# Optimization experiments

Measured on AMD Instinct MI355X. Metric: run time of the kernel, lower is better.

## Reference

```python
import jax, jax.numpy as jnp
import numpy as np

# LeNet-5 C3 connectivity table: which of the 6 input maps feed each of the 16 output maps.
MAP_S2 = [[0, 1, 2], [1, 2, 3], [2, 3, 4], [3, 4, 5], [0, 4, 5], [0, 1, 5],
          [0, 1, 2, 3], [1, 2, 3, 4], [2, 3, 4, 5], [0, 3, 4, 5], [0, 1, 4, 5],
          [0, 1, 2, 5], [0, 1, 3, 4], [1, 2, 4, 5], [0, 2, 3, 5], [0, 1, 2, 3, 4, 5]]

_mask_np = np.zeros((16, 6), dtype=np.float32)
for i, conn in enumerate(MAP_S2):
    _mask_np[i, conn] = 1.0
CONN_MASK = jnp.asarray(_mask_np)  # [out_ch=16, in_ch=6]


def setup_inputs() -> dict:
    key = jax.random.key(0)
    kx, kw, kb = jax.random.split(key, 3)
    x = jax.random.normal(kx, (32, 6, 512, 512), dtype=jnp.float32)
    # Dense weight; unconnected (out,in) pairs are masked to zero in reference(),
    # matching the per-output-channel gather + tiny conv of the original module.
    weight = jax.random.normal(kw, (16, 6, 5, 5), dtype=jnp.float32) * 0.1
    bias = jax.random.normal(kb, (16,), dtype=jnp.float32) * 0.1
    return {"x": x, "weight": weight, "bias": bias}


def reference(x, weight, bias):
    # Mask enforces the sparse channel connectivity: equivalent to gathering
    # each output map's input-channel subset and running a tiny 5x5 conv.
    w = weight * CONN_MASK[:, :, None, None]  # [16,6,5,5]
    out = jax.lax.conv_general_dilated(
        x, w,
        window_strides=(1, 1), padding='VALID',
        dimension_numbers=('NCHW', 'OIHW', 'NCHW'))
    return out + bias[None, :, None, None]  # [B,16,H-4,W-4]
```

## Files before the change

### kernel.cpp

```cpp
#include <hip/hip_runtime.h>


#define TILE_W 64
#define TILE_H 16
#define IN_W   (TILE_W + 4)
#define IN_H   (TILE_H + 4)

__global__ __launch_bounds__(256, 3) void c3_kernel(
    const float* __restrict__ x, const float* __restrict__ wgt,
    const float* __restrict__ bias, float* __restrict__ out)
{
    constexpr int IC = 6, OC = 16, H = 512, W = 512, OH = 508, OW = 508;
    static constexpr int CONN[6][10] = {
        {0, 4, 5, 6, 9, 10, 11, 12, 14, 15},
        {0, 1, 5, 6, 7, 10, 11, 12, 13, 15},
        {0, 1, 2, 6, 7, 8, 11, 13, 14, 15},
        {1, 2, 3, 6, 7, 8, 9, 12, 14, 15},
        {2, 3, 4, 7, 8, 9, 10, 12, 13, 15},
        {3, 4, 5, 8, 9, 10, 11, 13, 14, 15}};

    __shared__ __align__(16) float xs[IC][IN_H][IN_W];
    __shared__ __align__(16) float ws[IC][5][OC][8];

    const int tid = threadIdx.x;
    const int ow0 = blockIdx.x * TILE_W;
    const int oh0 = blockIdx.y * TILE_H;
    const int n   = blockIdx.z;

    for (int i = tid; i < OC * IC * 25; i += 256) {
        const int oc = i / 150;
        const int rem = i % 150;
        const int ic = rem / 25;
        const int kh = (rem % 25) / 5;
        const int kw = rem % 5;
        ws[ic][kh][oc][kw] = wgt[i];
    }

    const float* xn = x + (size_t)n * IC * H * W;
    for (int i = tid; i < IC * IN_H * (IN_W / 4); i += 256) {
        const int ic  = i / (IN_H * 17);
        const int rem = i % (IN_H * 17);
        const int r   = rem / 17;
        const int c4  = (rem % 17) * 4;
        int h = oh0 + r; if (h > H - 1) h = H - 1;
        const int wc = ow0 + c4;
        float4 v;
        if (wc <= W - 4) {
            v = *(const float4*)(xn + ((size_t)ic * H + h) * W + wc);
        } else {
            v = make_float4(0.f, 0.f, 0.f, 0.f);
        }
        *(float4*)&xs[ic][r][c4] = v;
    }
    __syncthreads();

    const int row = tid >> 4;
    const int c0  = (tid & 15) * 4;

    float acc[OC][4];
    #pragma unroll
    for (int oc = 0; oc < OC; ++oc)
        #pragma unroll
        for (int r = 0; r < 4; ++r) acc[oc][r] = 0.f;

    #pragma unroll 1
    for (int kh = 0; kh < 5; ++kh) {
        #pragma unroll
        for (int ic = 0; ic < IC; ++ic) {
            float in[8];
            *(float4*)&in[0] = *(const float4*)&xs[ic][row + kh][c0];
            *(float4*)&in[4] = *(const float4*)&xs[ic][row + kh][c0 + 4];
            #pragma unroll
            for (int j = 0; j < 10; ++j) {
                const int oc = CONN[ic][j];
                float wv[5];
                *(float4*)&wv[0] = *(const float4*)&ws[ic][kh][oc][0];
                wv[4] = ws[ic][kh][oc][4];
                #pragma unroll
                for (int kw = 0; kw < 5; ++kw)
                    #pragma unroll
                    for (int r = 0; r < 4; ++r)
                        acc[oc][r] = fmaf(in[r + kw], wv[kw], acc[oc][r]);
            }
        }
    }

    const int oh = oh0 + row;
    const int ow = ow0 + c0;
    if (oh < OH && ow < OW) {
        float* op = out + (((size_t)n * OC) * OH + oh) * OW + ow;
        #pragma unroll
        for (int oc = 0; oc < OC; ++oc) {
            const float b = bias[oc];
            float4 v = make_float4(acc[oc][0] + b, acc[oc][1] + b,
                                   acc[oc][2] + b, acc[oc][3] + b);
            *(float4*)(op + (size_t)oc * OH * OW) = v;
        }
    }
}

extern "C" void kernel_launch(void* const* d_in, const int* in_sizes, int n_in,
                              void* d_out, int out_size, void* d_ws, size_t ws_size,
                              hipStream_t stream) {
    const float* x    = (const float*)d_in[0];
    const float* wgt  = (const float*)d_in[1];
    const float* bias = (const float*)d_in[2];
    float* out = (float*)d_out;
    dim3 grid((508 + TILE_W - 1) / TILE_W,
              (508 + TILE_H - 1) / TILE_H,
              32);
    c3_kernel<<<grid, dim3(256), 0, stream>>>(x, wgt, bias, out);
}
```

Before: 965.0 us.

## Repack sparse weights in a prelaunch kernel and read them as uniform scalar loads

Adds a small one-block kernel that repacks only the connected weights into a contiguous per-(ic,kh) layout in workspace. The main kernel then reads weights straight from global memory with wave-uniform addresses, which should lower to scalar loads, instead of staging all weights in LDS. This drops the LDS weight buffer and its per-FMA LDS reads, and raises the occupancy hint to 4 blocks per CU. In exchange it adds an extra kernel launch and relies on the scalar cache for weight fetches.

```diff
diff --git a/kernel.cpp b/kernel.cpp
--- a/kernel.cpp
+++ b/kernel.cpp
@@ -6,35 +6,46 @@
 #define IN_W   (TILE_W + 4)
 #define IN_H   (TILE_H + 4)
 
-__global__ __launch_bounds__(256, 3) void c3_kernel(
-    const float* __restrict__ x, const float* __restrict__ wgt,
+#define CONN_TABLE {                              \
+    {0, 4, 5, 6, 9, 10, 11, 12, 14, 15},          \
+    {0, 1, 5, 6, 7, 10, 11, 12, 13, 15},          \
+    {0, 1, 2, 6, 7, 8, 11, 13, 14, 15},           \
+    {1, 2, 3, 6, 7, 8, 9, 12, 14, 15},            \
+    {2, 3, 4, 7, 8, 9, 10, 12, 13, 15},           \
+    {3, 4, 5, 8, 9, 10, 11, 13, 14, 15}}
+
+__global__ __launch_bounds__(256) void c3_repack(
+    const float* __restrict__ wgt, float* __restrict__ rp)
+{
+    static constexpr int CONN[6][10] = CONN_TABLE;
+    for (int idx = threadIdx.x; idx < 6 * 5 * 64; idx += 256) {
+        const int blk  = idx >> 6;
+        const int slot = idx & 63;
+        const int ic = blk / 5, kh = blk % 5;
+        float v = 0.f;
+        if (slot < 50) {
+            const int j = slot / 5, kw = slot % 5;
+            const int oc = CONN[ic][j];
+            v = wgt[((oc * 6 + ic) * 5 + kh) * 5 + kw];
+        }
+        rp[idx] = v;
+    }
+}
+
+template <bool PACKED>
+__global__ __launch_bounds__(256, 4) void c3_kernel(
+    const float* __restrict__ x, const float* __restrict__ wsrc,
     const float* __restrict__ bias, float* __restrict__ out)
 {
     constexpr int IC = 6, OC = 16, H = 512, W = 512, OH = 508, OW = 508;
-    static constexpr int CONN[6][10] = {
-        {0, 4, 5, 6, 9, 10, 11, 12, 14, 15},
-        {0, 1, 5, 6, 7, 10, 11, 12, 13, 15},
-        {0, 1, 2, 6, 7, 8, 11, 13, 14, 15},
-        {1, 2, 3, 6, 7, 8, 9, 12, 14, 15},
-        {2, 3, 4, 7, 8, 9, 10, 12, 13, 15},
-        {3, 4, 5, 8, 9, 10, 11, 13, 14, 15}};
+    static constexpr int CONN[6][10] = CONN_TABLE;
 
     __shared__ __align__(16) float xs[IC][IN_H][IN_W];
-    __shared__ __align__(16) float ws[IC][5][OC][8];
 
     const int tid = threadIdx.x;
     const int ow0 = blockIdx.x * TILE_W;
     const int oh0 = blockIdx.y * TILE_H;
     const int n   = blockIdx.z;
-
-    for (int i = tid; i < OC * IC * 25; i += 256) {
-        const int oc = i / 150;
-        const int rem = i % 150;
-        const int ic = rem / 25;
-        const int kh = (rem % 25) / 5;
-        const int kw = rem % 5;
-        ws[ic][kh][oc][kw] = wgt[i];
-    }
 
     const float* xn = x + (size_t)n * IC * H * W;
     for (int i = tid; i < IC * IN_H * (IN_W / 4); i += 256) {
@@ -73,14 +84,15 @@
             #pragma unroll
             for (int j = 0; j < 10; ++j) {
                 const int oc = CONN[ic][j];
-                float wv[5];
-                *(float4*)&wv[0] = *(const float4*)&ws[ic][kh][oc][0];
-                wv[4] = ws[ic][kh][oc][4];
                 #pragma unroll
-                for (int kw = 0; kw < 5; ++kw)
+                for (int kw = 0; kw < 5; ++kw) {
+                    const float wv = PACKED
+                        ? wsrc[(ic * 5 + kh) * 64 + j * 5 + kw]
+                        : wsrc[((oc * 6 + ic) * 5 + kh) * 5 + kw];
                     #pragma unroll
                     for (int r = 0; r < 4; ++r)
-                        acc[oc][r] = fmaf(in[r + kw], wv[kw], acc[oc][r]);
+                        acc[oc][r] = fmaf(in[r + kw], wv, acc[oc][r]);
+                }
             }
         }
     }
@@ -109,5 +121,11 @@
     dim3 grid((508 + TILE_W - 1) / TILE_W,
               (508 + TILE_H - 1) / TILE_H,
               32);
-    c3_kernel<<<grid, dim3(256), 0, stream>>>(x, wgt, bias, out);
+    if (ws_size >= 6 * 5 * 64 * sizeof(float)) {
+        c3_repack<<<dim3(1), dim3(256), 0, stream>>>(wgt, (float*)d_ws);
+        c3_kernel<true><<<grid, dim3(256), 0, stream>>>(
+            x, (const float*)d_ws, bias, out);
+    } else {
+        c3_kernel<false><<<grid, dim3(256), 0, stream>>>(x, wgt, bias, out);
+    }
 }
```

Measured after the change: 779.6 us. -19.2%, faster.
